# Performance work log

Measured on AMD Instinct MI355X. Metric: run time of the kernel, lower is better.

The kernel has to match this reference:

```python
import jax, jax.numpy as jnp
import numpy as np

H, W = 128, 128
SIGMAINV = 7000.0   # DIB-R default soft-silhouette sharpness
EPS = 1e-10


def _seg_d2(px, py, ax, ay, bx, by):
    # squared distance from pixel (px,py) [H,W] to segment a-b (each [B,F,1,1])
    abx = bx - ax; aby = by - ay
    apx = px - ax; apy = py - ay
    t = jnp.clip((apx * abx + apy * aby) / (abx * abx + aby * aby + EPS), 0.0, 1.0)
    dx = apx - t * abx; dy = apy - t * aby
    return dx * dx + dy * dy


def _rasterize(p3d, p2d, normalz, color12):
    # p3d: [B,F,9] camera-space verts, p2d: [B,F,6] screen verts, color12: [B,F,12]
    B, F = p2d.shape[:2]
    xs = (jnp.arange(W, dtype=jnp.float32) + 0.5) / W * 2.0 - 1.0
    ys = 1.0 - (jnp.arange(H, dtype=jnp.float32) + 0.5) / H * 2.0
    px = jnp.broadcast_to(xs[None, :], (H, W))
    py = jnp.broadcast_to(ys[:, None], (H, W))
    x0 = p2d[..., 0][..., None, None]; y0 = p2d[..., 1][..., None, None]
    x1 = p2d[..., 2][..., None, None]; y1 = p2d[..., 3][..., None, None]
    x2 = p2d[..., 4][..., None, None]; y2 = p2d[..., 5][..., None, None]
    area = (x1 - x0) * (y2 - y0) - (x2 - x0) * (y1 - y0)        # [B,F,1,1]
    denom = jnp.where(jnp.abs(area) > EPS, area, EPS)
    w0 = ((x1 - px) * (y2 - py) - (x2 - px) * (y1 - py)) / denom  # [B,F,H,W]
    w1 = ((x2 - px) * (y0 - py) - (x0 - px) * (y2 - py)) / denom
    w2 = 1.0 - w0 - w1
    front = (normalz[..., 0] > 0)[..., None, None]               # [B,F,1,1]
    valid = jnp.abs(area) > EPS
    inside = (w0 >= 0) & (w1 >= 0) & (w2 >= 0) & front & valid   # [B,F,H,W]
    z0 = p3d[..., 2][..., None, None]
    z1 = p3d[..., 5][..., None, None]
    z2 = p3d[..., 8][..., None, None]
    z = w0 * z0 + w1 * z1 + w2 * z2
    zbuf = jnp.where(inside, z, jnp.inf)
    fidx = jnp.argmin(zbuf, axis=1)                              # [B,H,W] nearest face
    hit = jnp.any(inside, axis=1)                                # [B,H,W]
    idx = fidx[:, None]                                          # [B,1,H,W]
    w0s = jnp.take_along_axis(w0, idx, axis=1)[:, 0]
    w1s = jnp.take_along_axis(w1, idx, axis=1)[:, 0]
    w2s = jnp.take_along_axis(w2, idx, axis=1)[:, 0]
    colsel = jax.vmap(lambda c, i: c[i])(color12, fidx)          # [B,H,W,12]
    feat = (w0s[..., None] * colsel[..., 0:4]
            + w1s[..., None] * colsel[..., 4:8]
            + w2s[..., None] * colsel[..., 8:12])
    feat = jnp.where(hit[..., None], feat, 0.0)                  # [B,H,W,4]
    d2 = jnp.minimum(jnp.minimum(_seg_d2(px, py, x0, y0, x1, y1),
                                 _seg_d2(px, py, x1, y1, x2, y2)),
                     _seg_d2(px, py, x2, y2, x0, y0))
    d2 = jnp.where(inside, 0.0, d2)
    probf = jnp.where(front & valid, jnp.exp(-d2 * SIGMAINV), 0.0)
    improb = 1.0 - jnp.prod(1.0 - probf, axis=1)                 # [B,H,W]
    return feat, improb[..., None]


def setup_inputs() -> dict:
    key = jax.random.key(0)
    k1, k2, k3 = jax.random.split(key, 3)
    B, P, F = 1, 256, 512
    points_bxpx3 = jax.random.normal(k1, (B, P, 3), jnp.float32) * 0.5
    colors_bxpx3 = jax.random.uniform(k2, (B, P, 3), jnp.float32)
    camera_rot_bx3x3 = jnp.broadcast_to(jnp.eye(3, dtype=jnp.float32), (B, 3, 3))
    camera_pos_bx3 = jnp.tile(jnp.array([[0.0, 0.0, -3.0]], dtype=jnp.float32), (B, 1))
    camera_proj_3x1 = jnp.array([[2.5], [2.5], [1.0]], dtype=jnp.float32)
    faces_fx3 = jax.random.randint(k3, (F, 3), 0, P, dtype=jnp.int32)
    return {"points_bxpx3": points_bxpx3, "colors_bxpx3": colors_bxpx3,
            "camera_rot_bx3x3": camera_rot_bx3x3, "camera_pos_bx3": camera_pos_bx3,
            "camera_proj_3x1": camera_proj_3x1, "faces_fx3": faces_fx3}


def reference(points_bxpx3, colors_bxpx3, camera_rot_bx3x3, camera_pos_bx3,
              camera_proj_3x1, faces_fx3):
    # perspective projection
    pts = points_bxpx3 - camera_pos_bx3[:, None, :]
    cam = jnp.einsum('bpk,bjk->bpj', pts, camera_rot_bx3x3)      # points @ rot^T
    proj = camera_proj_3x1.reshape(1, 1, 3)
    xy3 = cam * proj
    xy2 = xy3[..., :2] / xy3[..., 2:3]
    pf = cam[:, faces_fx3]                                       # [B,F,3,3]
    p3d = pf.reshape(pf.shape[0], pf.shape[1], 9)
    p2 = xy2[:, faces_fx3]                                       # [B,F,3,2]
    p2d = p2.reshape(p2.shape[0], p2.shape[1], 6)
    normal = jnp.cross(pf[:, :, 1] - pf[:, :, 0], pf[:, :, 2] - pf[:, :, 0])
    normalz = normal[..., 2:3]
    nlen = jnp.sqrt(jnp.sum(normal ** 2, axis=2, keepdims=True) + 1e-08)
    normal1 = normal / (nlen + 1e-15)
    cf = colors_bxpx3[:, faces_fx3]                              # [B,F,3,3]
    ones = jnp.ones_like(cf[:, :, 0, :1])
    color12 = jnp.concatenate([cf[:, :, 0], ones, cf[:, :, 1], ones,
                               cf[:, :, 2], ones], axis=2)       # [B,F,12]
    imfeat, improb = _rasterize(p3d, p2d, normalz, color12)
    imrender = imfeat[..., :3]
    return imrender, improb, normal1
```

## Files before the change

### kernel.cpp

```cpp
#include <hip/hip_runtime.h>
#include <math.h>

#define FF 512
#define SIGMAINV 7000.0f
#define EPSF 1e-10f
#define NW 8
#define FPW (FF / NW)

__global__ __launch_bounds__(512, 1) void vcrender_kernel(
    const float* __restrict__ points,
    const float* __restrict__ colors,
    const float* __restrict__ rot,
    const float* __restrict__ cpos,
    const float* __restrict__ proj,
    const int*   __restrict__ faces,
    float* __restrict__ out)
{
#pragma clang fp contract(off)
    __shared__ float sface[FF * 24];
    __shared__ float redz[NW * 64];
    __shared__ int   redi[NW * 64];
    __shared__ float redp[NW * 64];

    const int tid = threadIdx.x;

    {
        const int f = tid;
        const int i0 = faces[f * 3 + 0];
        const int i1 = faces[f * 3 + 1];
        const int i2 = faces[f * 3 + 2];
        const float r00 = rot[0], r01 = rot[1], r02 = rot[2];
        const float r10 = rot[3], r11 = rot[4], r12 = rot[5];
        const float r20 = rot[6], r21 = rot[7], r22 = rot[8];
        const float cx = cpos[0], cy = cpos[1], cz = cpos[2];
        const float pjx = proj[0], pjy = proj[1], pjz = proj[2];

        float camx[3], camy[3], camz[3], sx[3], sy[3];
        const int vidx[3] = {i0, i1, i2};
        for (int k = 0; k < 3; ++k) {
            const int vi = vidx[k];
            const float ax = points[vi * 3 + 0] - cx;
            const float ay = points[vi * 3 + 1] - cy;
            const float az = points[vi * 3 + 2] - cz;
            const float X = r00 * ax + r01 * ay + r02 * az;
            const float Y = r10 * ax + r11 * ay + r12 * az;
            const float Z = r20 * ax + r21 * ay + r22 * az;
            camx[k] = X; camy[k] = Y; camz[k] = Z;
            const float zz = Z * pjz;
            sx[k] = (X * pjx) / zz;
            sy[k] = (Y * pjy) / zz;
        }
        const float e1x = camx[1] - camx[0], e1y = camy[1] - camy[0], e1z = camz[1] - camz[0];
        const float e2x = camx[2] - camx[0], e2y = camy[2] - camy[0], e2z = camz[2] - camz[0];
        const float nx = e1y * e2z - e1z * e2y;
        const float ny = e1z * e2x - e1x * e2z;
        const float nz = e1x * e2y - e1y * e2x;
        const float nlen = sqrtf(nx * nx + ny * ny + nz * nz + 1e-8f);
        const float ninv = 1.0f / (nlen + 1e-15f);
        if (blockIdx.x == 0) {
            out[65536 + f * 3 + 0] = nx * ninv;
            out[65536 + f * 3 + 1] = ny * ninv;
            out[65536 + f * 3 + 2] = nz * ninv;
        }
        const float x0 = sx[0], y0 = sy[0], x1 = sx[1], y1 = sy[1], x2 = sx[2], y2 = sy[2];
        const float area = (x1 - x0) * (y2 - y0) - (x2 - x0) * (y1 - y0);
        const bool valid = fabsf(area) > EPSF;
        const float denom = valid ? area : EPSF;
        const float invd = 1.0f / denom;
        const bool fv = (nz > 0.0f) && valid;

        float* r = &sface[f * 24];
        r[0] = x0; r[1] = y0; r[2] = x1; r[3] = y1; r[4] = x2; r[5] = y2;
        r[6] = camz[0]; r[7] = camz[1]; r[8] = camz[2];
        r[9] = invd; r[10] = fv ? 1.0f : 0.0f;
        const float ab0x = x1 - x0, ab0y = y1 - y0;
        const float ab1x = x2 - x1, ab1y = y2 - y1;
        const float ab2x = x0 - x2, ab2y = y0 - y2;
        r[11] = ab0x; r[12] = ab0y; r[13] = 1.0f / (ab0x * ab0x + ab0y * ab0y + EPSF);
        r[14] = ab1x; r[15] = ab1y; r[16] = 1.0f / (ab1x * ab1x + ab1y * ab1y + EPSF);
        r[17] = ab2x; r[18] = ab2y; r[19] = 1.0f / (ab2x * ab2x + ab2y * ab2y + EPSF);
        const float RM = 0.0660f;
        float bx0, bx1, by0, by1;
        if (fv) {
            bx0 = fminf(fminf(x0, x1), x2) - RM;
            bx1 = fmaxf(fmaxf(x0, x1), x2) + RM;
            by0 = fminf(fminf(y0, y1), y2) - RM;
            by1 = fmaxf(fmaxf(y0, y1), y2) + RM;
        } else {
            bx0 = 1e30f; bx1 = -1e30f; by0 = 1e30f; by1 = -1e30f;
        }
        r[20] = bx0; r[21] = bx1; r[22] = by0; r[23] = by1;
    }
    __syncthreads();

    const int wv   = tid >> 6;
    const int lane = tid & 63;
    const int pix  = blockIdx.x * 64 + lane;
    const float px = ((pix & 127) + 0.5f) * (2.0f / 128.0f) - 1.0f;
    const float py = 1.0f - ((pix >> 7) + 0.5f) * (2.0f / 128.0f);

    float zmin = INFINITY;
    int   fmin = 0;
    float prod = 1.0f;

    const int fbeg = wv * FPW;
    for (int f = fbeg; f < fbeg + FPW; ++f) {
        const float* r = &sface[f * 24];
        const float bx0 = r[20], bx1 = r[21], by0 = r[22], by1 = r[23];
        if (px >= bx0 && px <= bx1 && py >= by0 && py <= by1) {
            const float x0 = r[0], y0 = r[1], x1 = r[2], y1 = r[3], x2 = r[4], y2 = r[5];
            const float invd = r[9];
            const float w0 = ((x1 - px) * (y2 - py) - (x2 - px) * (y1 - py)) * invd;
            const float w1 = ((x2 - px) * (y0 - py) - (x0 - px) * (y2 - py)) * invd;
            const float w2 = 1.0f - w0 - w1;
            const bool inside = (w0 >= 0.0f) && (w1 >= 0.0f) && (w2 >= 0.0f);
            const float z = w0 * r[6] + w1 * r[7] + w2 * r[8];
            if (inside && z < zmin) { zmin = z; fmin = f; }
            float apx, apy, t, dx, dy;
            apx = px - x0; apy = py - y0;
            t = fminf(fmaxf((apx * r[11] + apy * r[12]) * r[13], 0.0f), 1.0f);
            dx = apx - t * r[11]; dy = apy - t * r[12];
            float d2 = dx * dx + dy * dy;
            apx = px - x1; apy = py - y1;
            t = fminf(fmaxf((apx * r[14] + apy * r[15]) * r[16], 0.0f), 1.0f);
            dx = apx - t * r[14]; dy = apy - t * r[15];
            d2 = fminf(d2, dx * dx + dy * dy);
            apx = px - x2; apy = py - y2;
            t = fminf(fmaxf((apx * r[17] + apy * r[18]) * r[19], 0.0f), 1.0f);
            dx = apx - t * r[17]; dy = apy - t * r[18];
            d2 = fminf(d2, dx * dx + dy * dy);
            d2 = inside ? 0.0f : d2;
            prod *= (1.0f - __expf(-d2 * SIGMAINV));
        }
    }

    redz[wv * 64 + lane] = zmin;
    redi[wv * 64 + lane] = fmin;
    redp[wv * 64 + lane] = prod;
    __syncthreads();

    if (wv == 0) {
        float z = zmin; int fi = fmin; float pr = prod;
        for (int c = 1; c < NW; ++c) {
            const float zc = redz[c * 64 + lane];
            const float pc = redp[c * 64 + lane];
            const int   ic = redi[c * 64 + lane];
            if (zc < z) { z = zc; fi = ic; }
            pr *= pc;
        }
        float fr = 0.0f, fg = 0.0f, fb = 0.0f;
        if (z < INFINITY) {
            const float* r = &sface[fi * 24];
            const float x0 = r[0], y0 = r[1], x1 = r[2], y1 = r[3], x2 = r[4], y2 = r[5];
            const float invd = r[9];
            const float w0 = ((x1 - px) * (y2 - py) - (x2 - px) * (y1 - py)) * invd;
            const float w1 = ((x2 - px) * (y0 - py) - (x0 - px) * (y2 - py)) * invd;
            const float w2 = 1.0f - w0 - w1;
            const int i0 = faces[fi * 3 + 0], i1 = faces[fi * 3 + 1], i2 = faces[fi * 3 + 2];
            fr = w0 * colors[i0 * 3 + 0] + w1 * colors[i1 * 3 + 0] + w2 * colors[i2 * 3 + 0];
            fg = w0 * colors[i0 * 3 + 1] + w1 * colors[i1 * 3 + 1] + w2 * colors[i2 * 3 + 1];
            fb = w0 * colors[i0 * 3 + 2] + w1 * colors[i1 * 3 + 2] + w2 * colors[i2 * 3 + 2];
        }
        out[pix * 3 + 0] = fr;
        out[pix * 3 + 1] = fg;
        out[pix * 3 + 2] = fb;
        out[3 * 16384 + pix] = 1.0f - pr;
    }
}

extern "C" void kernel_launch(void* const* d_in, const int* in_sizes, int n_in,
                              void* d_out, int out_size, void* d_ws, size_t ws_size,
                              hipStream_t stream) {
    const float* points = (const float*)d_in[0];
    const float* colors = (const float*)d_in[1];
    const float* rot    = (const float*)d_in[2];
    const float* cpos   = (const float*)d_in[3];
    const float* proj   = (const float*)d_in[4];
    const int*   faces  = (const int*)d_in[5];
    float* out = (float*)d_out;
    vcrender_kernel<<<256, 512, 0, stream>>>(points, colors, rot, cpos, proj, faces, out);
}
```

Baseline: 77.56 us.

## Split per-face setup into a separate kernel writing face records to workspace

Moves the per-face projection and setup out of every raster block into a single-block setup kernel. That kernel writes 32-float face records, now including the gathered vertex colors, to the workspace. The raster kernel then reads face data straight from global memory with a wave-uniform index, so the loads can be scalar, rather than staging it in shared memory. This removes the setup work that all 256 blocks repeated and the shared-memory barrier, at the cost of a second kernel launch and a serialized single-block setup stage.

```diff
diff --git a/kernel.cpp b/kernel.cpp
--- a/kernel.cpp
+++ b/kernel.cpp
@@ -6,94 +6,98 @@
 #define EPSF 1e-10f
 #define NW 8
 #define FPW (FF / NW)
+#define RSTRIDE 32
 
-__global__ __launch_bounds__(512, 1) void vcrender_kernel(
+
+__global__ __launch_bounds__(512, 1) void vc_setup_kernel(
     const float* __restrict__ points,
     const float* __restrict__ colors,
     const float* __restrict__ rot,
     const float* __restrict__ cpos,
     const float* __restrict__ proj,
     const int*   __restrict__ faces,
+    float* __restrict__ out,
+    float* __restrict__ ws)
+{
+#pragma clang fp contract(off)
+    const int f = threadIdx.x;
+    const int i0 = faces[f * 3 + 0];
+    const int i1 = faces[f * 3 + 1];
+    const int i2 = faces[f * 3 + 2];
+    const float r00 = rot[0], r01 = rot[1], r02 = rot[2];
+    const float r10 = rot[3], r11 = rot[4], r12 = rot[5];
+    const float r20 = rot[6], r21 = rot[7], r22 = rot[8];
+    const float cx = cpos[0], cy = cpos[1], cz = cpos[2];
+    const float pjx = proj[0], pjy = proj[1], pjz = proj[2];
+
+    float camx[3], camy[3], camz[3], sx[3], sy[3];
+    const int vidx[3] = {i0, i1, i2};
+    for (int k = 0; k < 3; ++k) {
+        const int vi = vidx[k];
+        const float ax = points[vi * 3 + 0] - cx;
+        const float ay = points[vi * 3 + 1] - cy;
+        const float az = points[vi * 3 + 2] - cz;
+        const float X = r00 * ax + r01 * ay + r02 * az;
+        const float Y = r10 * ax + r11 * ay + r12 * az;
+        const float Z = r20 * ax + r21 * ay + r22 * az;
+        camx[k] = X; camy[k] = Y; camz[k] = Z;
+        const float zz = Z * pjz;
+        sx[k] = (X * pjx) / zz;
+        sy[k] = (Y * pjy) / zz;
+    }
+    const float e1x = camx[1] - camx[0], e1y = camy[1] - camy[0], e1z = camz[1] - camz[0];
+    const float e2x = camx[2] - camx[0], e2y = camy[2] - camy[0], e2z = camz[2] - camz[0];
+    const float nx = e1y * e2z - e1z * e2y;
+    const float ny = e1z * e2x - e1x * e2z;
+    const float nz = e1x * e2y - e1y * e2x;
+    const float nlen = sqrtf(nx * nx + ny * ny + nz * nz + 1e-8f);
+    const float ninv = 1.0f / (nlen + 1e-15f);
+    out[65536 + f * 3 + 0] = nx * ninv;
+    out[65536 + f * 3 + 1] = ny * ninv;
+    out[65536 + f * 3 + 2] = nz * ninv;
+
+    const float x0 = sx[0], y0 = sy[0], x1 = sx[1], y1 = sy[1], x2 = sx[2], y2 = sy[2];
+    const float area = (x1 - x0) * (y2 - y0) - (x2 - x0) * (y1 - y0);
+    const bool valid = fabsf(area) > EPSF;
+    const float denom = valid ? area : EPSF;
+    const float invd = 1.0f / denom;
+    const bool fv = (nz > 0.0f) && valid;
+
+    float* r = &ws[f * RSTRIDE];
+    const float RM = 0.0660f;
+    if (fv) {
+        r[0] = fminf(fminf(x0, x1), x2) - RM;
+        r[1] = fmaxf(fmaxf(x0, x1), x2) + RM;
+        r[2] = fminf(fminf(y0, y1), y2) - RM;
+        r[3] = fmaxf(fmaxf(y0, y1), y2) + RM;
+    } else {
+        r[0] = 1e30f; r[1] = -1e30f; r[2] = 1e30f; r[3] = -1e30f;
+    }
+    r[4] = x0; r[5] = y0; r[6] = x1; r[7] = y1; r[8] = x2; r[9] = y2;
+    r[10] = camz[0]; r[11] = camz[1]; r[12] = camz[2];
+    r[13] = invd;
+    const float ab0x = x1 - x0, ab0y = y1 - y0;
+    const float ab1x = x2 - x1, ab1y = y2 - y1;
+    const float ab2x = x0 - x2, ab2y = y0 - y2;
+    r[14] = ab0x; r[15] = ab0y; r[16] = 1.0f / (ab0x * ab0x + ab0y * ab0y + EPSF);
+    r[17] = ab1x; r[18] = ab1y; r[19] = 1.0f / (ab1x * ab1x + ab1y * ab1y + EPSF);
+    r[20] = ab2x; r[21] = ab2y; r[22] = 1.0f / (ab2x * ab2x + ab2y * ab2y + EPSF);
+    r[23] = colors[i0 * 3 + 0]; r[24] = colors[i0 * 3 + 1]; r[25] = colors[i0 * 3 + 2];
+    r[26] = colors[i1 * 3 + 0]; r[27] = colors[i1 * 3 + 1]; r[28] = colors[i1 * 3 + 2];
+    r[29] = colors[i2 * 3 + 0]; r[30] = colors[i2 * 3 + 1]; r[31] = colors[i2 * 3 + 2];
+}
+
+__global__ __launch_bounds__(512, 1) void vc_raster_kernel(
+    const float* __restrict__ ws,
     float* __restrict__ out)
 {
 #pragma clang fp contract(off)
-    __shared__ float sface[FF * 24];
     __shared__ float redz[NW * 64];
     __shared__ int   redi[NW * 64];
     __shared__ float redp[NW * 64];
 
-    const int tid = threadIdx.x;
-
-    {
-        const int f = tid;
-        const int i0 = faces[f * 3 + 0];
-        const int i1 = faces[f * 3 + 1];
-        const int i2 = faces[f * 3 + 2];
-        const float r00 = rot[0], r01 = rot[1], r02 = rot[2];
-        const float r10 = rot[3], r11 = rot[4], r12 = rot[5];
-        const float r20 = rot[6], r21 = rot[7], r22 = rot[8];
-        const float cx = cpos[0], cy = cpos[1], cz = cpos[2];
-        const float pjx = proj[0], pjy = proj[1], pjz = proj[2];
-
-        float camx[3], camy[3], camz[3], sx[3], sy[3];
-        const int vidx[3] = {i0, i1, i2};
-        for (int k = 0; k < 3; ++k) {
-            const int vi = vidx[k];
-            const float ax = points[vi * 3 + 0] - cx;
-            const float ay = points[vi * 3 + 1] - cy;
-            const float az = points[vi * 3 + 2] - cz;
-            const float X = r00 * ax + r01 * ay + r02 * az;
-            const float Y = r10 * ax + r11 * ay + r12 * az;
-            const float Z = r20 * ax + r21 * ay + r22 * az;
-            camx[k] = X; camy[k] = Y; camz[k] = Z;
-            const float zz = Z * pjz;
-            sx[k] = (X * pjx) / zz;
-            sy[k] = (Y * pjy) / zz;
-        }
-        const float e1x = camx[1] - camx[0], e1y = camy[1] - camy[0], e1z = camz[1] - camz[0];
-        const float e2x = camx[2] - camx[0], e2y = camy[2] - camy[0], e2z = camz[2] - camz[0];
-        const float nx = e1y * e2z - e1z * e2y;
-        const float ny = e1z * e2x - e1x * e2z;
-        const float nz = e1x * e2y - e1y * e2x;
-        const float nlen = sqrtf(nx * nx + ny * ny + nz * nz + 1e-8f);
-        const float ninv = 1.0f / (nlen + 1e-15f);
-        if (blockIdx.x == 0) {
-            out[65536 + f * 3 + 0] = nx * ninv;
-            out[65536 + f * 3 + 1] = ny * ninv;
-            out[65536 + f * 3 + 2] = nz * ninv;
-        }
-        const float x0 = sx[0], y0 = sy[0], x1 = sx[1], y1 = sy[1], x2 = sx[2], y2 = sy[2];
-        const float area = (x1 - x0) * (y2 - y0) - (x2 - x0) * (y1 - y0);
-        const bool valid = fabsf(area) > EPSF;
-        const float denom = valid ? area : EPSF;
-        const float invd = 1.0f / denom;
-        const bool fv = (nz > 0.0f) && valid;
-
-        float* r = &sface[f * 24];
-        r[0] = x0; r[1] = y0; r[2] = x1; r[3] = y1; r[4] = x2; r[5] = y2;
-        r[6] = camz[0]; r[7] = camz[1]; r[8] = camz[2];
-        r[9] = invd; r[10] = fv ? 1.0f : 0.0f;
-        const float ab0x = x1 - x0, ab0y = y1 - y0;
-        const float ab1x = x2 - x1, ab1y = y2 - y1;
-        const float ab2x = x0 - x2, ab2y = y0 - y2;
-        r[11] = ab0x; r[12] = ab0y; r[13] = 1.0f / (ab0x * ab0x + ab0y * ab0y + EPSF);
-        r[14] = ab1x; r[15] = ab1y; r[16] = 1.0f / (ab1x * ab1x + ab1y * ab1y + EPSF);
-        r[17] = ab2x; r[18] = ab2y; r[19] = 1.0f / (ab2x * ab2x + ab2y * ab2y + EPSF);
-        const float RM = 0.0660f;
-        float bx0, bx1, by0, by1;
-        if (fv) {
-            bx0 = fminf(fminf(x0, x1), x2) - RM;
-            bx1 = fmaxf(fmaxf(x0, x1), x2) + RM;
-            by0 = fminf(fminf(y0, y1), y2) - RM;
-            by1 = fmaxf(fmaxf(y0, y1), y2) + RM;
-        } else {
-            bx0 = 1e30f; bx1 = -1e30f; by0 = 1e30f; by1 = -1e30f;
-        }
-        r[20] = bx0; r[21] = bx1; r[22] = by0; r[23] = by1;
-    }
-    __syncthreads();
-
-    const int wv   = tid >> 6;
+    const int tid  = threadIdx.x;
+    const int wv   = __builtin_amdgcn_readfirstlane(tid >> 6);
     const int lane = tid & 63;
     const int pix  = blockIdx.x * 64 + lane;
     const float px = ((pix & 127) + 0.5f) * (2.0f / 128.0f) - 1.0f;
@@ -105,29 +109,29 @@
 
     const int fbeg = wv * FPW;
     for (int f = fbeg; f < fbeg + FPW; ++f) {
-        const float* r = &sface[f * 24];
-        const float bx0 = r[20], bx1 = r[21], by0 = r[22], by1 = r[23];
+        const float* r = &ws[f * RSTRIDE];
+        const float bx0 = r[0], bx1 = r[1], by0 = r[2], by1 = r[3];
         if (px >= bx0 && px <= bx1 && py >= by0 && py <= by1) {
-            const float x0 = r[0], y0 = r[1], x1 = r[2], y1 = r[3], x2 = r[4], y2 = r[5];
-            const float invd = r[9];
+            const float x0 = r[4], y0 = r[5], x1 = r[6], y1 = r[7], x2 = r[8], y2 = r[9];
+            const float invd = r[13];
             const float w0 = ((x1 - px) * (y2 - py) - (x2 - px) * (y1 - py)) * invd;
             const float w1 = ((x2 - px) * (y0 - py) - (x0 - px) * (y2 - py)) * invd;
             const float w2 = 1.0f - w0 - w1;
             const bool inside = (w0 >= 0.0f) && (w1 >= 0.0f) && (w2 >= 0.0f);
-            const float z = w0 * r[6] + w1 * r[7] + w2 * r[8];
+            const float z = w0 * r[10] + w1 * r[11] + w2 * r[12];
             if (inside && z < zmin) { zmin = z; fmin = f; }
             float apx, apy, t, dx, dy;
             apx = px - x0; apy = py - y0;
-            t = fminf(fmaxf((apx * r[11] + apy * r[12]) * r[13], 0.0f), 1.0f);
-            dx = apx - t * r[11]; dy = apy - t * r[12];
+            t = fminf(fmaxf((apx * r[14] + apy * r[15]) * r[16], 0.0f), 1.0f);
+            dx = apx - t * r[14]; dy = apy - t * r[15];
             float d2 = dx * dx + dy * dy;
             apx = px - x1; apy = py - y1;
-            t = fminf(fmaxf((apx * r[14] + apy * r[15]) * r[16], 0.0f), 1.0f);
-            dx = apx - t * r[14]; dy = apy - t * r[15];
+            t = fminf(fmaxf((apx * r[17] + apy * r[18]) * r[19], 0.0f), 1.0f);
+            dx = apx - t * r[17]; dy = apy - t * r[18];
             d2 = fminf(d2, dx * dx + dy * dy);
             apx = px - x2; apy = py - y2;
-            t = fminf(fmaxf((apx * r[17] + apy * r[18]) * r[19], 0.0f), 1.0f);
-            dx = apx - t * r[17]; dy = apy - t * r[18];
+            t = fminf(fmaxf((apx * r[20] + apy * r[21]) * r[22], 0.0f), 1.0f);
+            dx = apx - t * r[20]; dy = apy - t * r[21];
             d2 = fminf(d2, dx * dx + dy * dy);
             d2 = inside ? 0.0f : d2;
             prod *= (1.0f - __expf(-d2 * SIGMAINV));
@@ -150,16 +154,15 @@
         }
         float fr = 0.0f, fg = 0.0f, fb = 0.0f;
         if (z < INFINITY) {
-            const float* r = &sface[fi * 24];
-            const float x0 = r[0], y0 = r[1], x1 = r[2], y1 = r[3], x2 = r[4], y2 = r[5];
-            const float invd = r[9];
+            const float* r = &ws[fi * RSTRIDE];
+            const float x0 = r[4], y0 = r[5], x1 = r[6], y1 = r[7], x2 = r[8], y2 = r[9];
+            const float invd = r[13];
             const float w0 = ((x1 - px) * (y2 - py) - (x2 - px) * (y1 - py)) * invd;
             const float w1 = ((x2 - px) * (y0 - py) - (x0 - px) * (y2 - py)) * invd;
             const float w2 = 1.0f - w0 - w1;
-            const int i0 = faces[fi * 3 + 0], i1 = faces[fi * 3 + 1], i2 = faces[fi * 3 + 2];
-            fr = w0 * colors[i0 * 3 + 0] + w1 * colors[i1 * 3 + 0] + w2 * colors[i2 * 3 + 0];
-            fg = w0 * colors[i0 * 3 + 1] + w1 * colors[i1 * 3 + 1] + w2 * colors[i2 * 3 + 1];
-            fb = w0 * colors[i0 * 3 + 2] + w1 * colors[i1 * 3 + 2] + w2 * colors[i2 * 3 + 2];
+            fr = w0 * r[23] + w1 * r[26] + w2 * r[29];
+            fg = w0 * r[24] + w1 * r[27] + w2 * r[30];
+            fb = w0 * r[25] + w1 * r[28] + w2 * r[31];
         }
         out[pix * 3 + 0] = fr;
         out[pix * 3 + 1] = fg;
@@ -178,5 +181,7 @@
     const float* proj   = (const float*)d_in[4];
     const int*   faces  = (const int*)d_in[5];
     float* out = (float*)d_out;
-    vcrender_kernel<<<256, 512, 0, stream>>>(points, colors, rot, cpos, proj, faces, out);
+    float* ws  = (float*)d_ws;
+    vc_setup_kernel<<<1, 512, 0, stream>>>(points, colors, rot, cpos, proj, faces, out, ws);
+    vc_raster_kernel<<<256, 512, 0, stream>>>(ws, out);
 }
```

Result: slower. 89.30 us (+15.1%).

## Compact faces per block row via ballot culling and balance across waves

Applied to the files above, without the earlier changes.

Each block now culls faces against its 64-pixel row span with a wave ballot and prefix sum, writing only surviving faces into a compact float4 shared-memory list. Waves then split that compacted list evenly instead of fixed 64-face ranges. Inside pixels skip the edge-distance computation by setting prod to zero directly. This adds two extra barriers and a serial prefix step, but it aims to remove most per-pixel bbox tests and the load imbalance between waves.

```diff
diff --git a/kernel.cpp b/kernel.cpp
--- a/kernel.cpp
+++ b/kernel.cpp
@@ -5,7 +5,8 @@
 #define SIGMAINV 7000.0f
 #define EPSF 1e-10f
 #define NW 8
-#define FPW (FF / NW)
+#define RMF 0.0660f
+
 
 __global__ __launch_bounds__(512, 1) void vcrender_kernel(
     const float* __restrict__ points,
@@ -17,15 +18,27 @@
     float* __restrict__ out)
 {
 #pragma clang fp contract(off)
-    __shared__ float sface[FF * 24];
-    __shared__ float redz[NW * 64];
-    __shared__ int   redi[NW * 64];
-    __shared__ float redp[NW * 64];
-
-    const int tid = threadIdx.x;
-
+    __shared__ float4 srec[FF * 4];
+    __shared__ int    scount[NW];
+    __shared__ int    sbase[NW];
+    __shared__ int    stotal;
+    __shared__ float  redz[NW * 64];
+    __shared__ int    redi[NW * 64];
+    __shared__ float  redp[NW * 64];
+
+    const int tid  = threadIdx.x;
+    const int lane = tid & 63;
+    const int wv   = tid >> 6;
+
+    const int   pixbase = blockIdx.x * 64;
+    const float py    = 1.0f - ((pixbase >> 7) + 0.5f) * (2.0f / 128.0f);
+    const float pxmin = ((pixbase & 127) + 0.5f) * (2.0f / 128.0f) - 1.0f;
+    const float pxmax = ((pixbase & 127) + 63 + 0.5f) * (2.0f / 128.0f) - 1.0f;
+
+    bool  flag = false;
+    float4 q0, q1, q2, q3;
     {
-        const int f = tid;
+        const int f  = tid;
         const int i0 = faces[f * 3 + 0];
         const int i1 = faces[f * 3 + 1];
         const int i2 = faces[f * 3 + 2];
@@ -69,94 +82,117 @@
         const float invd = 1.0f / denom;
         const bool fv = (nz > 0.0f) && valid;
 
-        float* r = &sface[f * 24];
-        r[0] = x0; r[1] = y0; r[2] = x1; r[3] = y1; r[4] = x2; r[5] = y2;
-        r[6] = camz[0]; r[7] = camz[1]; r[8] = camz[2];
-        r[9] = invd; r[10] = fv ? 1.0f : 0.0f;
+        const float bx0 = fminf(fminf(x0, x1), x2) - RMF;
+        const float bx1 = fmaxf(fmaxf(x0, x1), x2) + RMF;
+        const float by0 = fminf(fminf(y0, y1), y2) - RMF;
+        const float by1 = fmaxf(fmaxf(y0, y1), y2) + RMF;
+        flag = fv && (by0 <= py) && (by1 >= py) && (bx0 <= pxmax) && (bx1 >= pxmin);
+
         const float ab0x = x1 - x0, ab0y = y1 - y0;
         const float ab1x = x2 - x1, ab1y = y2 - y1;
         const float ab2x = x0 - x2, ab2y = y0 - y2;
-        r[11] = ab0x; r[12] = ab0y; r[13] = 1.0f / (ab0x * ab0x + ab0y * ab0y + EPSF);
-        r[14] = ab1x; r[15] = ab1y; r[16] = 1.0f / (ab1x * ab1x + ab1y * ab1y + EPSF);
-        r[17] = ab2x; r[18] = ab2y; r[19] = 1.0f / (ab2x * ab2x + ab2y * ab2y + EPSF);
-        const float RM = 0.0660f;
-        float bx0, bx1, by0, by1;
-        if (fv) {
-            bx0 = fminf(fminf(x0, x1), x2) - RM;
-            bx1 = fmaxf(fmaxf(x0, x1), x2) + RM;
-            by0 = fminf(fminf(y0, y1), y2) - RM;
-            by1 = fmaxf(fmaxf(y0, y1), y2) + RM;
-        } else {
-            bx0 = 1e30f; bx1 = -1e30f; by0 = 1e30f; by1 = -1e30f;
-        }
-        r[20] = bx0; r[21] = bx1; r[22] = by0; r[23] = by1;
-    }
-    __syncthreads();
-
-    const int wv   = tid >> 6;
-    const int lane = tid & 63;
-    const int pix  = blockIdx.x * 64 + lane;
+        q0 = make_float4(bx0, bx1, invd, camz[0]);
+        q1 = make_float4(x0, y0, x1, y1);
+        q2 = make_float4(x2, y2, camz[1], camz[2]);
+        q3 = make_float4(1.0f / (ab0x * ab0x + ab0y * ab0y + EPSF),
+                         1.0f / (ab1x * ab1x + ab1y * ab1y + EPSF),
+                         1.0f / (ab2x * ab2x + ab2y * ab2y + EPSF),
+                         __int_as_float(f));
+    }
+    const unsigned long long mask = __ballot(flag);
+    if (lane == 0) scount[wv] = __popcll(mask);
+    __syncthreads();
+    if (tid == 0) {
+        int s = 0;
+        for (int i = 0; i < NW; ++i) { sbase[i] = s; s += scount[i]; }
+        stotal = s;
+    }
+    __syncthreads();
+    if (flag) {
+        const int pos = sbase[wv] + __popcll(mask & ((1ull << lane) - 1ull));
+        srec[pos * 4 + 0] = q0;
+        srec[pos * 4 + 1] = q1;
+        srec[pos * 4 + 2] = q2;
+        srec[pos * 4 + 3] = q3;
+    }
+    __syncthreads();
+    const int n = stotal;
+
+    const int pix = pixbase + lane;
     const float px = ((pix & 127) + 0.5f) * (2.0f / 128.0f) - 1.0f;
-    const float py = 1.0f - ((pix >> 7) + 0.5f) * (2.0f / 128.0f);
 
     float zmin = INFINITY;
-    int   fmin = 0;
+    int   smin = 0;
     float prod = 1.0f;
 
-    const int fbeg = wv * FPW;
-    for (int f = fbeg; f < fbeg + FPW; ++f) {
-        const float* r = &sface[f * 24];
-        const float bx0 = r[20], bx1 = r[21], by0 = r[22], by1 = r[23];
-        if (px >= bx0 && px <= bx1 && py >= by0 && py <= by1) {
-            const float x0 = r[0], y0 = r[1], x1 = r[2], y1 = r[3], x2 = r[4], y2 = r[5];
-            const float invd = r[9];
+    const int chunk = (n + NW - 1) >> 3;
+    const int fbeg = wv * chunk;
+    const int fend = min(fbeg + chunk, n);
+    for (int s = fbeg; s < fend; ++s) {
+        const float4 b = srec[s * 4 + 0];
+        if (px >= b.x && px <= b.y) {
+            const float4 v01 = srec[s * 4 + 1];
+            const float4 v2z = srec[s * 4 + 2];
+            const float x0 = v01.x, y0 = v01.y, x1 = v01.z, y1 = v01.w;
+            const float x2 = v2z.x, y2 = v2z.y;
+            const float invd = b.z;
             const float w0 = ((x1 - px) * (y2 - py) - (x2 - px) * (y1 - py)) * invd;
             const float w1 = ((x2 - px) * (y0 - py) - (x0 - px) * (y2 - py)) * invd;
             const float w2 = 1.0f - w0 - w1;
-            const bool inside = (w0 >= 0.0f) && (w1 >= 0.0f) && (w2 >= 0.0f);
-            const float z = w0 * r[6] + w1 * r[7] + w2 * r[8];
-            if (inside && z < zmin) { zmin = z; fmin = f; }
-            float apx, apy, t, dx, dy;
-            apx = px - x0; apy = py - y0;
-            t = fminf(fmaxf((apx * r[11] + apy * r[12]) * r[13], 0.0f), 1.0f);
-            dx = apx - t * r[11]; dy = apy - t * r[12];
-            float d2 = dx * dx + dy * dy;
-            apx = px - x1; apy = py - y1;
-            t = fminf(fmaxf((apx * r[14] + apy * r[15]) * r[16], 0.0f), 1.0f);
-            dx = apx - t * r[14]; dy = apy - t * r[15];
-            d2 = fminf(d2, dx * dx + dy * dy);
-            apx = px - x2; apy = py - y2;
-            t = fminf(fmaxf((apx * r[17] + apy * r[18]) * r[19], 0.0f), 1.0f);
-            dx = apx - t * r[17]; dy = apy - t * r[18];
-            d2 = fminf(d2, dx * dx + dy * dy);
-            d2 = inside ? 0.0f : d2;
-            prod *= (1.0f - __expf(-d2 * SIGMAINV));
+            const float z = w0 * b.w + w1 * v2z.z + w2 * v2z.w;
+            if (w0 >= 0.0f && w1 >= 0.0f && w2 >= 0.0f) {
+                if (z < zmin) { zmin = z; smin = s; }
+                prod = 0.0f;
+            } else {
+                const float4 ei = srec[s * 4 + 3];
+                const float ab0x = x1 - x0, ab0y = y1 - y0;
+                const float ab1x = x2 - x1, ab1y = y2 - y1;
+                const float ab2x = x0 - x2, ab2y = y0 - y2;
+                float apx, apy, t, dx, dy;
+                apx = px - x0; apy = py - y0;
+                t = fminf(fmaxf((apx * ab0x + apy * ab0y) * ei.x, 0.0f), 1.0f);
+                dx = apx - t * ab0x; dy = apy - t * ab0y;
+                float d2 = dx * dx + dy * dy;
+                apx = px - x1; apy = py - y1;
+                t = fminf(fmaxf((apx * ab1x + apy * ab1y) * ei.y, 0.0f), 1.0f);
+                dx = apx - t * ab1x; dy = apy - t * ab1y;
+                d2 = fminf(d2, dx * dx + dy * dy);
+                apx = px - x2; apy = py - y2;
+                t = fminf(fmaxf((apx * ab2x + apy * ab2y) * ei.z, 0.0f), 1.0f);
+                dx = apx - t * ab2x; dy = apy - t * ab2y;
+                d2 = fminf(d2, dx * dx + dy * dy);
+                prod *= (1.0f - __expf(-d2 * SIGMAINV));
+            }
         }
     }
 
     redz[wv * 64 + lane] = zmin;
-    redi[wv * 64 + lane] = fmin;
+    redi[wv * 64 + lane] = smin;
     redp[wv * 64 + lane] = prod;
     __syncthreads();
 
     if (wv == 0) {
-        float z = zmin; int fi = fmin; float pr = prod;
+        float z = zmin; int si = smin; float pr = prod;
         for (int c = 1; c < NW; ++c) {
             const float zc = redz[c * 64 + lane];
             const float pc = redp[c * 64 + lane];
             const int   ic = redi[c * 64 + lane];
-            if (zc < z) { z = zc; fi = ic; }
+            if (zc < z) { z = zc; si = ic; }
             pr *= pc;
         }
         float fr = 0.0f, fg = 0.0f, fb = 0.0f;
         if (z < INFINITY) {
-            const float* r = &sface[fi * 24];
-            const float x0 = r[0], y0 = r[1], x1 = r[2], y1 = r[3], x2 = r[4], y2 = r[5];
-            const float invd = r[9];
+            const float4 b   = srec[si * 4 + 0];
+            const float4 v01 = srec[si * 4 + 1];
+            const float4 v2z = srec[si * 4 + 2];
+            const float x0 = v01.x, y0 = v01.y, x1 = v01.z, y1 = v01.w;
+            const float x2 = v2z.x, y2 = v2z.y;
+            const float invd = b.z;
             const float w0 = ((x1 - px) * (y2 - py) - (x2 - px) * (y1 - py)) * invd;
             const float w1 = ((x2 - px) * (y0 - py) - (x0 - px) * (y2 - py)) * invd;
             const float w2 = 1.0f - w0 - w1;
-            const int i0 = faces[fi * 3 + 0], i1 = faces[fi * 3 + 1], i2 = faces[fi * 3 + 2];
+            const int fid = __float_as_int(srec[si * 4 + 3].w);
+            const int i0 = faces[fid * 3 + 0], i1 = faces[fid * 3 + 1], i2 = faces[fid * 3 + 2];
             fr = w0 * colors[i0 * 3 + 0] + w1 * colors[i1 * 3 + 0] + w2 * colors[i2 * 3 + 0];
             fg = w0 * colors[i0 * 3 + 1] + w1 * colors[i1 * 3 + 1] + w2 * colors[i2 * 3 + 1];
             fb = w0 * colors[i0 * 3 + 2] + w1 * colors[i1 * 3 + 2] + w2 * colors[i2 * 3 + 2];
```

Measured after the change: 74.84 us. 3.5% less time.
